# Performance work log

Hardware: AMD Instinct MI355X
Metric: run time of the kernel (lower is better)

The kernel has to match this reference:

```python
import jax, jax.numpy as jnp
import numpy as np

N = 100000   # nodes (word + doc)
E = 1600000  # edges
IN = 256     # in_feats
H = 64       # n_hidden
MH = 64      # mlp_hidden
C = 16       # n_classes


def setup_inputs() -> dict:
    key = jax.random.key(0)
    ks = jax.random.split(key, 12)
    s = lambda f: 1.0 / np.sqrt(f)
    return {
        "x": jax.random.normal(ks[0], (N, IN), jnp.float32),
        "edge_index": jax.random.randint(ks[1], (2, E), 0, N, dtype=jnp.int64),
        "edge_weight": jax.random.uniform(ks[2], (E,), jnp.float32),
        "W1": jax.random.normal(ks[3], (IN, H), jnp.float32) * s(IN),
        "b1": jnp.zeros((H,), jnp.float32),
        "W2": jax.random.normal(ks[4], (H, H), jnp.float32) * s(H),
        "b2": jnp.zeros((H,), jnp.float32),
        "Wm1": jax.random.normal(ks[5], (H, MH), jnp.float32) * s(H),
        "bm1": jnp.zeros((MH,), jnp.float32),
        "Wm2": jax.random.normal(ks[6], (MH, C), jnp.float32) * s(MH),
        "bm2": jnp.zeros((C,), jnp.float32),
    }


def _gcn_norm(edge_index, edge_weight, n):
    # PyG GCNConv: add self-loops (weight 1), symmetric normalization
    loops = jnp.arange(n, dtype=edge_index.dtype)
    src = jnp.concatenate([edge_index[0], loops])
    dst = jnp.concatenate([edge_index[1], loops])
    w = jnp.concatenate([edge_weight, jnp.ones((n,), edge_weight.dtype)])
    deg = jax.ops.segment_sum(w, dst, num_segments=n)
    dinv = jnp.where(deg > 0, jax.lax.rsqrt(deg), 0.0)
    norm = dinv[src] * w * dinv[dst]
    return src, dst, norm


def _gcn_conv(x, W, b, src, dst, norm, n):
    h = x @ W                           # [N, out]
    msg = h[src] * norm[:, None]        # gather + scale, [E+N, out]
    agg = jax.ops.segment_sum(msg, dst, num_segments=n)
    return agg + b


def reference(x, edge_index, edge_weight, W1, b1, W2, b2, Wm1, bm1, Wm2, bm2):
    src, dst, norm = _gcn_norm(edge_index, edge_weight, N)
    # GCN stack (eval mode: dropout is identity)
    h = jax.nn.relu(_gcn_conv(x, W1, b1, src, dst, norm, N))
    h = jax.nn.relu(_gcn_conv(h, W2, b2, src, dst, norm, N))
    # MLP head
    h = jax.nn.relu(h @ Wm1 + bm1)
    logits = h @ Wm2 + bm2
    return jax.nn.softmax(logits, axis=-1)
```

## Files before the change

### kernel.cpp

```cpp
#include <hip/hip_runtime.h>
#include <cstdint>
#include <cstddef>

#define NN 100000
#define NE 1600000
#define IN_F 256
#define HD 64
#define NC 16

#define NT 391
#define NBLK 196
#define EPB 8192
#define CM (NT * NBLK)
#define SCB 75



__global__ __launch_bounds__(256) void k_count(const int* __restrict__ dstA,
                                               int* __restrict__ counts) {
    __shared__ int hist[NT];
    int tid = threadIdx.x;
    for (int t = tid; t < NT; t += 256) hist[t] = 0;
    __syncthreads();
    int base = blockIdx.x * EPB;
#pragma unroll
    for (int i = 0; i < 32; ++i) {
        int e = base + i * 256 + tid;
        if (e < NE) atomicAdd(&hist[dstA[e] >> 8], 1);
    }
    __syncthreads();
    for (int t = tid; t < NT; t += 256)
        counts[t * NBLK + blockIdx.x] = hist[t];
}

__global__ __launch_bounds__(256) void k_scan1(int* __restrict__ c,
                                               int* __restrict__ bsum) {
    __shared__ int ss[256];
    int t = threadIdx.x;
    int base = blockIdx.x * 1024 + t * 4;
    int c0 = (base + 0 < CM) ? c[base + 0] : 0;
    int c1 = (base + 1 < CM) ? c[base + 1] : 0;
    int c2 = (base + 2 < CM) ? c[base + 2] : 0;
    int c3 = (base + 3 < CM) ? c[base + 3] : 0;
    int tsum = c0 + c1 + c2 + c3;
    ss[t] = tsum;
    __syncthreads();
    for (int off = 1; off < 256; off <<= 1) {
        int v = (t >= off) ? ss[t - off] : 0;
        __syncthreads();
        ss[t] += v;
        __syncthreads();
    }
    int excl = ss[t] - tsum;
    if (t == 255) bsum[blockIdx.x] = ss[255];
    if (base + 0 < CM) c[base + 0] = excl;
    if (base + 1 < CM) c[base + 1] = excl + c0;
    if (base + 2 < CM) c[base + 2] = excl + c0 + c1;
    if (base + 3 < CM) c[base + 3] = excl + c0 + c1 + c2;
}

__global__ __launch_bounds__(128) void k_scan2(const int* __restrict__ bsum,
                                               int* __restrict__ bpref) {
    __shared__ int ss[128];
    int t = threadIdx.x;
    int v = (t < SCB) ? bsum[t] : 0;
    ss[t] = v;
    __syncthreads();
    for (int off = 1; off < 128; off <<= 1) {
        int u = (t >= off) ? ss[t - off] : 0;
        __syncthreads();
        ss[t] += u;
        __syncthreads();
    }
    if (t < SCB) bpref[t] = ss[t] - v;
}

__global__ __launch_bounds__(256) void k_scan3(int* __restrict__ c,
                                               const int* __restrict__ bpref) {
    int i = blockIdx.x * 256 + threadIdx.x;
    if (i < CM) c[i] += bpref[i >> 10];
}

template <bool FULL>
__global__ __launch_bounds__(256) void k_fill2(const int* __restrict__ srcA,
                                               const int* __restrict__ dstA,
                                               const float* __restrict__ ew,
                                               const int* __restrict__ counts,
                                               int2* __restrict__ tmp) {
    __shared__ int basel[NT];
    int tid = threadIdx.x;
    for (int t = tid; t < NT; t += 256) basel[t] = counts[t * NBLK + blockIdx.x];
    __syncthreads();
    int eb = blockIdx.x * EPB;
#pragma unroll
    for (int i = 0; i < 32; ++i) {
        int e = eb + i * 256 + tid;
        if (e < NE) {
            int d = dstA[e];
            int pos = atomicAdd(&basel[d >> 8], 1);
            if (FULL)
                tmp[pos] = make_int2(srcA[e] | ((d & 255) << 17),
                                     __float_as_int(ew[e]));
            else
                tmp[pos] = make_int2(e, d & 255);
        }
    }
}

template <bool FULL>
__global__ __launch_bounds__(256) void k_sort(const int* __restrict__ counts,
                                              const int2* __restrict__ tmp,
                                              int2* __restrict__ outP,
                                              int* __restrict__ outE,
                                              int* __restrict__ rowptr,
                                              const float* __restrict__ ew,
                                              float* __restrict__ dinv) {
    __shared__ int hist[256], ss[256], bases[256];
    int tid = threadIdx.x;
    int tile = blockIdx.x;
    int bs = counts[tile * NBLK];
    int be = (tile + 1 < NT) ? counts[(tile + 1) * NBLK] : NE;
    hist[tid] = 0;
    __syncthreads();
    for (int p = bs + tid; p < be; p += 256) {
        int dl = FULL ? ((tmp[p].x >> 17) & 255) : tmp[p].y;
        atomicAdd(&hist[dl], 1);
    }
    __syncthreads();
    int v = hist[tid];
    ss[tid] = v;
    __syncthreads();
    for (int off = 1; off < 256; off <<= 1) {
        int u = (tid >= off) ? ss[tid - off] : 0;
        __syncthreads();
        ss[tid] += u;
        __syncthreads();
    }
    int excl = ss[tid] - v;
    bases[tid] = bs + excl;
    int row = tile * 256 + tid;
    if (row < NN) rowptr[row] = bs + excl;
    if (tile == NT - 1 && tid == 0) rowptr[NN] = NE;
    __syncthreads();
    for (int p = bs + tid; p < be; p += 256) {
        int2 t2 = tmp[p];
        int dl = FULL ? ((t2.x >> 17) & 255) : t2.y;
        int pos = atomicAdd(&bases[dl], 1);
        if (FULL) outP[pos] = t2;
        else      outE[pos] = t2.x;
    }
    __syncthreads();
    if (row < NN) {
        int p0 = bs + excl, p1 = bs + excl + v;
        float s = 1.0f;
        for (int p = p0; p < p1; ++p)
            s += FULL ? __int_as_float(outP[p].y) : ew[outE[p]];
        dinv[row] = rsqrtf(s);
    }
}

template <bool FULL>
__global__ __launch_bounds__(256) void k_agg(const int* __restrict__ rowptr,
                                             const int2* __restrict__ pairsS,
                                             const int* __restrict__ eid,
                                             const int* __restrict__ srcA,
                                             const float* __restrict__ ew,
                                             const float* __restrict__ dinv,
                                             const float* __restrict__ g,
                                             float* __restrict__ agg) {
    int row = blockIdx.x * 4 + (threadIdx.x >> 6);
    int lane = threadIdx.x & 63;
    if (row >= NN) return;
    int p = rowptr[row], pe = rowptr[row + 1];
    float di = dinv[row];
    float acc = g[(size_t)row * HD + lane];
    for (; p + 8 <= pe; p += 8) {
        int   sv[8];
        float wv[8];
        if (FULL) {
#pragma unroll
            for (int i = 0; i < 8; ++i) {
                int2 v = pairsS[p + i];
                sv[i] = v.x & 0x1FFFF;
                wv[i] = __int_as_float(v.y);
            }
        } else {
            int ev[8];
#pragma unroll
            for (int i = 0; i < 8; ++i) ev[i] = eid[p + i];
#pragma unroll
            for (int i = 0; i < 8; ++i) { sv[i] = srcA[ev[i]]; wv[i] = ew[ev[i]]; }
        }
        float gs[8];
#pragma unroll
        for (int i = 0; i < 8; ++i)
            gs[i] = g[(size_t)sv[i] * HD + lane];
#pragma unroll
        for (int i = 0; i < 8; ++i)
            acc = fmaf(wv[i], gs[i], acc);
    }
    for (; p + 4 <= pe; p += 4) {
        if (FULL) {
            int2 v0 = pairsS[p], v1 = pairsS[p + 1],
                 v2 = pairsS[p + 2], v3 = pairsS[p + 3];
            int s0 = v0.x & 0x1FFFF, s1 = v1.x & 0x1FFFF,
                s2 = v2.x & 0x1FFFF, s3 = v3.x & 0x1FFFF;
            float g0 = g[(size_t)s0 * HD + lane];
            float g1 = g[(size_t)s1 * HD + lane];
            float g2 = g[(size_t)s2 * HD + lane];
            float g3 = g[(size_t)s3 * HD + lane];
            acc = fmaf(__int_as_float(v0.y), g0, acc);
            acc = fmaf(__int_as_float(v1.y), g1, acc);
            acc = fmaf(__int_as_float(v2.y), g2, acc);
            acc = fmaf(__int_as_float(v3.y), g3, acc);
        } else {
            int e0 = eid[p], e1 = eid[p + 1], e2 = eid[p + 2], e3 = eid[p + 3];
            int s0 = srcA[e0], s1 = srcA[e1], s2 = srcA[e2], s3 = srcA[e3];
            float g0 = g[(size_t)s0 * HD + lane];
            float g1 = g[(size_t)s1 * HD + lane];
            float g2 = g[(size_t)s2 * HD + lane];
            float g3 = g[(size_t)s3 * HD + lane];
            acc = fmaf(ew[e0], g0, acc);
            acc = fmaf(ew[e1], g1, acc);
            acc = fmaf(ew[e2], g2, acc);
            acc = fmaf(ew[e3], g3, acc);
        }
    }
    for (; p < pe; ++p) {
        if (FULL) {
            int2 v = pairsS[p];
            acc = fmaf(__int_as_float(v.y),
                       g[(size_t)(v.x & 0x1FFFF) * HD + lane], acc);
        } else {
            int e = eid[p];
            acc = fmaf(ew[e], g[(size_t)srcA[e] * HD + lane], acc);
        }
    }
    agg[(size_t)row * HD + lane] = di * acc;
}

template <bool SCALE>
__global__ __launch_bounds__(256, 6) void k_gemm1(const float* __restrict__ x,
                                                  const float* __restrict__ W1,
                                                  const float* __restrict__ dinv,
                                                  float* __restrict__ h0) {
    __shared__ float sX[32][68];
    __shared__ float sW[32][64];
    int tid = threadIdx.x;
    int rs  = tid >> 4;
    int cg  = tid & 15;
    int base = blockIdx.x * 64;

    int f4   = tid >> 5;
    int srow = tid & 31;

    float acc[4][4];
#pragma unroll
    for (int r = 0; r < 4; ++r)
#pragma unroll
        for (int c = 0; c < 4; ++c) acc[r][c] = 0.0f;

    for (int kc = 0; kc < IN_F; kc += 32) {
        __syncthreads();
        {
            const float4* wsrc = (const float4*)(W1 + (size_t)kc * HD);
            float4* wdst = (float4*)&sW[0][0];
            wdst[tid]       = wsrc[tid];
            wdst[256 + tid] = wsrc[256 + tid];
        }
#pragma unroll
        for (int q = 0; q < 2; ++q) {
            int grow = q * 32 + srow;
            int growc = (base + grow < NN) ? (base + grow) : (NN - 1);
            float4 v = *(const float4*)(x + (size_t)growc * IN_F + kc + f4 * 4);
            sX[f4 * 4 + 0][grow] = v.x;
            sX[f4 * 4 + 1][grow] = v.y;
            sX[f4 * 4 + 2][grow] = v.z;
            sX[f4 * 4 + 3][grow] = v.w;
        }
        __syncthreads();
#pragma unroll 4
        for (int k = 0; k < 32; ++k) {
            float xs[4];
            *(float4*)xs = *(const float4*)&sX[k][rs * 4];
            float wv[4];
            *(float4*)wv = *(const float4*)&sW[k][cg * 4];
#pragma unroll
            for (int r = 0; r < 4; ++r) {
                float xj = xs[r];
#pragma unroll
                for (int c = 0; c < 4; ++c) acc[r][c] = fmaf(xj, wv[c], acc[r][c]);
            }
        }
    }
#pragma unroll
    for (int r = 0; r < 4; ++r) {
        int row = base + rs * 4 + r;
        if (row >= NN) continue;
        float di = SCALE ? dinv[row] : 1.0f;
        *(float4*)(h0 + (size_t)row * HD + cg * 4) =
            make_float4(acc[r][0] * di, acc[r][1] * di,
                        acc[r][2] * di, acc[r][3] * di);
    }
}

template <bool BIASRELU, bool SCALEOUT>
__global__ __launch_bounds__(256, 6) void k_gemm64(const float* __restrict__ in,
                                                   const float* __restrict__ bin,
                                                   const float* __restrict__ W,
                                                   const float* __restrict__ bout,
                                                   const float* __restrict__ dinv,
                                                   float* __restrict__ outA) {
    __shared__ float sW[HD * HD];
    __shared__ float sBin[HD];
    int tid = threadIdx.x;
    int rs  = tid >> 4;
    int cg  = tid & 15;
    int base = blockIdx.x * 64;
    int rowc[4];
    bool rv[4];
#pragma unroll
    for (int r = 0; r < 4; ++r) {
        int row = base + rs + 16 * r;
        rv[r] = row < NN;
        rowc[r] = rv[r] ? row : (NN - 1);
    }
    {
        const float4* wsrc = (const float4*)W;
        float4* wdst = (float4*)sW;
#pragma unroll
        for (int q = 0; q < 4; ++q) wdst[q * 256 + tid] = wsrc[q * 256 + tid];
        if (tid < 16) ((float4*)sBin)[tid] = ((const float4*)bin)[tid];
    }
    __syncthreads();
    float acc[4][4];
#pragma unroll
    for (int r = 0; r < 4; ++r)
#pragma unroll
        for (int c = 0; c < 4; ++c) acc[r][c] = 0.0f;

    for (int k4 = 0; k4 < 16; ++k4) {
        float bs[4];
        *(float4*)bs = ((const float4*)sBin)[k4];
        float xs[4][4];
#pragma unroll
        for (int r = 0; r < 4; ++r)
            *(float4*)xs[r] = *(const float4*)(in + (size_t)rowc[r] * HD + k4 * 4);
#pragma unroll
        for (int j = 0; j < 4; ++j) {
            float wv[4];
            *(float4*)wv = *(const float4*)(sW + (k4 * 4 + j) * HD + cg * 4);
#pragma unroll
            for (int r = 0; r < 4; ++r) {
                float hv = fmaxf(xs[r][j] + bs[j], 0.0f);
#pragma unroll
                for (int c = 0; c < 4; ++c) acc[r][c] = fmaf(hv, wv[c], acc[r][c]);
            }
        }
    }
#pragma unroll
    for (int r = 0; r < 4; ++r) {
        if (!rv[r]) continue;
        float* ha = outA + (size_t)rowc[r] * HD + cg * 4;
        if (BIASRELU) {
            float bo[4];
            *(float4*)bo = *(const float4*)(bout + cg * 4);
            *(float4*)ha = make_float4(fmaxf(acc[r][0] + bo[0], 0.0f),
                                       fmaxf(acc[r][1] + bo[1], 0.0f),
                                       fmaxf(acc[r][2] + bo[2], 0.0f),
                                       fmaxf(acc[r][3] + bo[3], 0.0f));
        } else {
            float di = SCALEOUT ? dinv[rowc[r]] : 1.0f;
            *(float4*)ha = make_float4(acc[r][0] * di, acc[r][1] * di,
                                       acc[r][2] * di, acc[r][3] * di);
        }
    }
}

__global__ __launch_bounds__(256) void k_init_fb(float* __restrict__ deg) {
    int i = blockIdx.x * 256 + threadIdx.x;
    if (i < NN) deg[i] = 1.0f;
}
__global__ __launch_bounds__(256) void k_edge_fb(const int* __restrict__ dst,
                                                 const float* __restrict__ ew,
                                                 float* __restrict__ deg) {
    int e = blockIdx.x * 256 + threadIdx.x;
    if (e < NE) atomicAdd(&deg[dst[e]], ew[e]);
}
__global__ __launch_bounds__(256) void k_dinv_fb(float* __restrict__ deg) {
    int i = blockIdx.x * 256 + threadIdx.x;
    if (i < NN) {
        float d = deg[i];
        deg[i] = d > 0.0f ? rsqrtf(d) : 0.0f;
    }
}
__global__ __launch_bounds__(256) void k_selfloop(const float* __restrict__ h,
                                                  const float* __restrict__ dinv,
                                                  float* __restrict__ agg) {
    int i = blockIdx.x * 256 + threadIdx.x;
    if (i >= NN * (HD / 4)) return;
    int row = i / (HD / 4);
    float di = dinv[row];
    float d2 = di * di;
    float4 v = ((const float4*)h)[i];
    ((float4*)agg)[i] = make_float4(v.x * d2, v.y * d2, v.z * d2, v.w * d2);
}
__global__ __launch_bounds__(256) void k_scatter(const int* __restrict__ src,
                                                 const int* __restrict__ dst,
                                                 const float* __restrict__ ew,
                                                 const float* __restrict__ dinv,
                                                 const float* __restrict__ h,
                                                 float* __restrict__ agg) {
    int e = blockIdx.x * 4 + (threadIdx.x >> 6);
    int lane = threadIdx.x & 63;
    if (e >= NE) return;
    int s = src[e];
    int d = dst[e];
    float nrm = dinv[s] * ew[e] * dinv[d];
    float v = h[(size_t)s * HD + lane] * nrm;
    atomicAdd(&agg[(size_t)d * HD + lane], v);
}

__global__ __launch_bounds__(256, 4) void k_out(const float* __restrict__ h3,
                                                const float* __restrict__ Wm2,
                                                const float* __restrict__ bm2,
                                                float* __restrict__ out) {
    __shared__ float sW[HD * NC];
    int tid = threadIdx.x;
    ((float4*)sW)[tid] = ((const float4*)Wm2)[tid];
    __syncthreads();
    int row = blockIdx.x * 256 + tid;
    bool rv = row < NN;
    int rowc = rv ? row : (NN - 1);
    float acc[16];
#pragma unroll
    for (int c = 0; c < 16; ++c) acc[c] = 0.0f;

    for (int k4 = 0; k4 < 16; ++k4) {
        float xs[4];
        *(float4*)xs = *(const float4*)(h3 + (size_t)rowc * HD + k4 * 4);
#pragma unroll
        for (int j = 0; j < 4; ++j) {
            float wv[16];
            const float4* wr4 = (const float4*)(sW + (k4 * 4 + j) * NC);
#pragma unroll
            for (int q = 0; q < 4; ++q) ((float4*)wv)[q] = wr4[q];
            float xj = xs[j];
#pragma unroll
            for (int c = 0; c < 16; ++c) acc[c] = fmaf(xj, wv[c], acc[c]);
        }
    }
    if (!rv) return;
    float bm[16];
#pragma unroll
    for (int q = 0; q < 4; ++q) ((float4*)bm)[q] = ((const float4*)bm2)[q];
    float l[16];
#pragma unroll
    for (int c = 0; c < 16; ++c) l[c] = acc[c] + bm[c];
    float m = l[0];
#pragma unroll
    for (int c = 1; c < 16; ++c) m = fmaxf(m, l[c]);
    float ssum = 0.0f;
#pragma unroll
    for (int c = 0; c < 16; ++c) {
        l[c] = expf(l[c] - m);
        ssum += l[c];
    }
    float inv = 1.0f / ssum;
    float4* op = (float4*)(out + (size_t)rowc * NC);
#pragma unroll
    for (int q = 0; q < 4; ++q)
        op[q] = make_float4(l[q * 4] * inv, l[q * 4 + 1] * inv,
                            l[q * 4 + 2] * inv, l[q * 4 + 3] * inv);
}

extern "C" void kernel_launch(void* const* d_in, const int* in_sizes, int n_in,
                              void* d_out, int out_size, void* d_ws, size_t ws_size,
                              hipStream_t stream) {
    const float* x   = (const float*)d_in[0];
    const int*   ei  = (const int*)d_in[1];
    const float* ew  = (const float*)d_in[2];
    const float* W1  = (const float*)d_in[3];
    const float* b1  = (const float*)d_in[4];
    const float* W2  = (const float*)d_in[5];
    const float* b2  = (const float*)d_in[6];
    const float* Wm1 = (const float*)d_in[7];
    const float* bm1 = (const float*)d_in[8];
    const float* Wm2 = (const float*)d_in[9];
    const float* bm2 = (const float*)d_in[10];
    float* out = (float*)d_out;

    char* base = (char*)d_ws;
    float* dinv   = (float*)base;
    float* A      = (float*)(base + 400128);
    float* B      = (float*)(base + 26000128);
    int*   rowptr = (int*)(base + 51600128);
    int2*  pairsS = (int2*)(base + 52000256);
    int2*  tmp    = (int2*)(base + 400128);
    int*   counts = (int*)(base + 26000128);
    int*   bsum   = (int*)(base + 26000128 + 306544);
    int*   bpref  = (int*)(base + 26000128 + 306944);

    const int* src = ei;
    const int* dst = ei + NE;

    const bool full  = ws_size >= (size_t)64800912;
    const bool douta = !full && ws_size >= (size_t)52000912;
    const int g_node = (NN + 255) / 256;
    const int g_g1   = (NN + 63) / 64;
    const int g_g64  = (NN + 63) / 64;
    const int g_agg  = (NN + 3) / 4;
    const int g_red  = (NN * (HD / 4) + 255) / 256;
    const int g_out  = (NN + 255) / 256;
    int* eid = (int*)d_out;

    if (full || douta) {
        k_count<<<dim3(NBLK), dim3(256), 0, stream>>>(dst, counts);
        k_scan1<<<dim3(SCB), dim3(256), 0, stream>>>(counts, bsum);
        k_scan2<<<dim3(1), dim3(128), 0, stream>>>(bsum, bpref);
        k_scan3<<<dim3((CM + 255) / 256), dim3(256), 0, stream>>>(counts, bpref);
        if (full) {
            k_fill2<true><<<dim3(NBLK), dim3(256), 0, stream>>>(src, dst, ew, counts, tmp);
            k_sort<true><<<dim3(NT), dim3(256), 0, stream>>>(counts, tmp, pairsS, nullptr, rowptr, ew, dinv);
        } else {
            k_fill2<false><<<dim3(NBLK), dim3(256), 0, stream>>>(src, dst, ew, counts, tmp);
            k_sort<false><<<dim3(NT), dim3(256), 0, stream>>>(counts, tmp, nullptr, eid, rowptr, ew, dinv);
        }
        k_gemm1<true><<<dim3(g_g1), dim3(256), 0, stream>>>(x, W1, dinv, A);
        if (full)
            k_agg<true><<<dim3(g_agg), dim3(256), 0, stream>>>(rowptr, pairsS, nullptr, src, ew, dinv, A, B);
        else
            k_agg<false><<<dim3(g_agg), dim3(256), 0, stream>>>(rowptr, nullptr, eid, src, ew, dinv, A, B);
        k_gemm64<false, true><<<dim3(g_g64), dim3(256), 0, stream>>>(B, b1, W2, nullptr, dinv, A);
        if (full)
            k_agg<true><<<dim3(g_agg), dim3(256), 0, stream>>>(rowptr, pairsS, nullptr, src, ew, dinv, A, B);
        else
            k_agg<false><<<dim3(g_agg), dim3(256), 0, stream>>>(rowptr, nullptr, eid, src, ew, dinv, A, B);
        k_gemm64<true, false><<<dim3(g_g64), dim3(256), 0, stream>>>(B, b2, Wm1, bm1, dinv, A);
        k_out<<<dim3(g_out), dim3(256), 0, stream>>>(A, Wm2, bm2, out);
    } else {
        k_init_fb<<<dim3(g_node), dim3(256), 0, stream>>>(dinv);
        k_edge_fb<<<dim3(NE / 256), dim3(256), 0, stream>>>(dst, ew, dinv);
        k_dinv_fb<<<dim3(g_node), dim3(256), 0, stream>>>(dinv);
        k_gemm1<false><<<dim3(g_g1), dim3(256), 0, stream>>>(x, W1, dinv, A);
        k_selfloop<<<dim3(g_red), dim3(256), 0, stream>>>(A, dinv, B);
        k_scatter<<<dim3(NE / 4), dim3(256), 0, stream>>>(src, dst, ew, dinv, A, B);
        k_gemm64<false, false><<<dim3(g_g64), dim3(256), 0, stream>>>(B, b1, W2, nullptr, dinv, A);
        k_selfloop<<<dim3(g_red), dim3(256), 0, stream>>>(A, dinv, B);
        k_scatter<<<dim3(NE / 4), dim3(256), 0, stream>>>(src, dst, ew, dinv, A, B);
        k_gemm64<true, false><<<dim3(g_g64), dim3(256), 0, stream>>>(B, b2, Wm1, bm1, dinv, A);
        k_out<<<dim3(g_out), dim3(256), 0, stream>>>(A, Wm2, bm2, out);
    }
}
```

Baseline: 479.3 us.

## Enlarge gemm1 per-thread tile and stage gemm64 inputs through shared memory

k_gemm1 now runs 128-thread blocks where each thread computes a 4x8 output tile instead of 4x4, so each shared-memory load feeds more FMAs, at the cost of more accumulator registers and fewer threads to hide latency. k_gemm64 now loads the 64x64 input tile once into transposed shared memory with bias+ReLU applied during staging, then runs an inner loop over shared memory. Previously each thread re-read inputs from global memory and recomputed the bias+ReLU per FMA group. The row mapping in gemm64 changes from strided to contiguous rows per thread, and its occupancy hint drops to 4 blocks.

```diff
diff --git a/kernel.cpp b/kernel.cpp
--- a/kernel.cpp
+++ b/kernel.cpp
@@ -240,56 +240,61 @@
 }
 
 template <bool SCALE>
-__global__ __launch_bounds__(256, 6) void k_gemm1(const float* __restrict__ x,
+__global__ __launch_bounds__(128, 3) void k_gemm1(const float* __restrict__ x,
                                                   const float* __restrict__ W1,
                                                   const float* __restrict__ dinv,
                                                   float* __restrict__ h0) {
     __shared__ float sX[32][68];
     __shared__ float sW[32][64];
     int tid = threadIdx.x;
-    int rs  = tid >> 4;
-    int cg  = tid & 15;
+    int rs  = tid >> 3;
+    int cg  = tid & 7;
     int base = blockIdx.x * 64;
 
     int f4   = tid >> 5;
     int srow = tid & 31;
 
-    float acc[4][4];
+    float acc[4][8];
 #pragma unroll
     for (int r = 0; r < 4; ++r)
 #pragma unroll
-        for (int c = 0; c < 4; ++c) acc[r][c] = 0.0f;
+        for (int c = 0; c < 8; ++c) acc[r][c] = 0.0f;
 
     for (int kc = 0; kc < IN_F; kc += 32) {
         __syncthreads();
         {
             const float4* wsrc = (const float4*)(W1 + (size_t)kc * HD);
             float4* wdst = (float4*)&sW[0][0];
-            wdst[tid]       = wsrc[tid];
-            wdst[256 + tid] = wsrc[256 + tid];
+#pragma unroll
+            for (int q = 0; q < 4; ++q) wdst[q * 128 + tid] = wsrc[q * 128 + tid];
         }
 #pragma unroll
         for (int q = 0; q < 2; ++q) {
             int grow = q * 32 + srow;
             int growc = (base + grow < NN) ? (base + grow) : (NN - 1);
-            float4 v = *(const float4*)(x + (size_t)growc * IN_F + kc + f4 * 4);
-            sX[f4 * 4 + 0][grow] = v.x;
-            sX[f4 * 4 + 1][grow] = v.y;
-            sX[f4 * 4 + 2][grow] = v.z;
-            sX[f4 * 4 + 3][grow] = v.w;
+#pragma unroll
+            for (int q2 = 0; q2 < 2; ++q2) {
+                int koff = q2 * 16 + f4 * 4;
+                float4 v = *(const float4*)(x + (size_t)growc * IN_F + kc + koff);
+                sX[koff + 0][grow] = v.x;
+                sX[koff + 1][grow] = v.y;
+                sX[koff + 2][grow] = v.z;
+                sX[koff + 3][grow] = v.w;
+            }
         }
         __syncthreads();
 #pragma unroll 4
         for (int k = 0; k < 32; ++k) {
             float xs[4];
             *(float4*)xs = *(const float4*)&sX[k][rs * 4];
-            float wv[4];
-            *(float4*)wv = *(const float4*)&sW[k][cg * 4];
+            float wv[8];
+            *(float4*)(wv + 0) = *(const float4*)&sW[k][cg * 8];
+            *(float4*)(wv + 4) = *(const float4*)&sW[k][cg * 8 + 4];
 #pragma unroll
             for (int r = 0; r < 4; ++r) {
                 float xj = xs[r];
 #pragma unroll
-                for (int c = 0; c < 4; ++c) acc[r][c] = fmaf(xj, wv[c], acc[r][c]);
+                for (int c = 0; c < 8; ++c) acc[r][c] = fmaf(xj, wv[c], acc[r][c]);
             }
         }
     }
@@ -298,70 +303,78 @@
         int row = base + rs * 4 + r;
         if (row >= NN) continue;
         float di = SCALE ? dinv[row] : 1.0f;
-        *(float4*)(h0 + (size_t)row * HD + cg * 4) =
-            make_float4(acc[r][0] * di, acc[r][1] * di,
-                        acc[r][2] * di, acc[r][3] * di);
+        float* hp = h0 + (size_t)row * HD + cg * 8;
+        *(float4*)(hp + 0) = make_float4(acc[r][0] * di, acc[r][1] * di,
+                                         acc[r][2] * di, acc[r][3] * di);
+        *(float4*)(hp + 4) = make_float4(acc[r][4] * di, acc[r][5] * di,
+                                         acc[r][6] * di, acc[r][7] * di);
     }
 }
 
 template <bool BIASRELU, bool SCALEOUT>
-__global__ __launch_bounds__(256, 6) void k_gemm64(const float* __restrict__ in,
+__global__ __launch_bounds__(256, 4) void k_gemm64(const float* __restrict__ in,
                                                    const float* __restrict__ bin,
                                                    const float* __restrict__ W,
                                                    const float* __restrict__ bout,
                                                    const float* __restrict__ dinv,
                                                    float* __restrict__ outA) {
-    __shared__ float sW[HD * HD];
-    __shared__ float sBin[HD];
+    __shared__ float sIn[64][68];
+    __shared__ float sW[64][64];
     int tid = threadIdx.x;
     int rs  = tid >> 4;
     int cg  = tid & 15;
     int base = blockIdx.x * 64;
-    int rowc[4];
-    bool rv[4];
-#pragma unroll
-    for (int r = 0; r < 4; ++r) {
-        int row = base + rs + 16 * r;
-        rv[r] = row < NN;
-        rowc[r] = rv[r] ? row : (NN - 1);
-    }
+    int f4   = tid >> 5;
+    int srow = tid & 31;
+
     {
         const float4* wsrc = (const float4*)W;
-        float4* wdst = (float4*)sW;
+        float4* wdst = (float4*)&sW[0][0];
 #pragma unroll
         for (int q = 0; q < 4; ++q) wdst[q * 256 + tid] = wsrc[q * 256 + tid];
-        if (tid < 16) ((float4*)sBin)[tid] = ((const float4*)bin)[tid];
-    }
-    __syncthreads();
+    }
+#pragma unroll
+    for (int q2 = 0; q2 < 2; ++q2) {
+        int koff = q2 * 32 + f4 * 4;
+        float4 bb = *(const float4*)(bin + koff);
+#pragma unroll
+        for (int q = 0; q < 2; ++q) {
+            int grow = q * 32 + srow;
+            int growc = (base + grow < NN) ? (base + grow) : (NN - 1);
+            float4 v = *(const float4*)(in + (size_t)growc * HD + koff);
+            sIn[koff + 0][grow] = fmaxf(v.x + bb.x, 0.0f);
+            sIn[koff + 1][grow] = fmaxf(v.y + bb.y, 0.0f);
+            sIn[koff + 2][grow] = fmaxf(v.z + bb.z, 0.0f);
+            sIn[koff + 3][grow] = fmaxf(v.w + bb.w, 0.0f);
+        }
+    }
+    __syncthreads();
+
     float acc[4][4];
 #pragma unroll
     for (int r = 0; r < 4; ++r)
 #pragma unroll
         for (int c = 0; c < 4; ++c) acc[r][c] = 0.0f;
 
-    for (int k4 = 0; k4 < 16; ++k4) {
-        float bs[4];
-        *(float4*)bs = ((const float4*)sBin)[k4];
-        float xs[4][4];
-#pragma unroll
-        for (int r = 0; r < 4; ++r)
-            *(float4*)xs[r] = *(const float4*)(in + (size_t)rowc[r] * HD + k4 * 4);
-#pragma unroll
-        for (int j = 0; j < 4; ++j) {
-            float wv[4];
-            *(float4*)wv = *(const float4*)(sW + (k4 * 4 + j) * HD + cg * 4);
-#pragma unroll
-            for (int r = 0; r < 4; ++r) {
-                float hv = fmaxf(xs[r][j] + bs[j], 0.0f);
-#pragma unroll
-                for (int c = 0; c < 4; ++c) acc[r][c] = fmaf(hv, wv[c], acc[r][c]);
-            }
-        }
-    }
+#pragma unroll 4
+    for (int k = 0; k < HD; ++k) {
+        float xs[4];
+        *(float4*)xs = *(const float4*)&sIn[k][rs * 4];
+        float wv[4];
+        *(float4*)wv = *(const float4*)&sW[k][cg * 4];
+#pragma unroll
+        for (int r = 0; r < 4; ++r) {
+            float hv = xs[r];
+#pragma unroll
+            for (int c = 0; c < 4; ++c) acc[r][c] = fmaf(hv, wv[c], acc[r][c]);
+        }
+    }
+
 #pragma unroll
     for (int r = 0; r < 4; ++r) {
-        if (!rv[r]) continue;
-        float* ha = outA + (size_t)rowc[r] * HD + cg * 4;
+        int row = base + rs * 4 + r;
+        if (row >= NN) continue;
+        float* ha = outA + (size_t)row * HD + cg * 4;
         if (BIASRELU) {
             float bo[4];
             *(float4*)bo = *(const float4*)(bout + cg * 4);
@@ -370,7 +383,7 @@
                                        fmaxf(acc[r][2] + bo[2], 0.0f),
                                        fmaxf(acc[r][3] + bo[3], 0.0f));
         } else {
-            float di = SCALEOUT ? dinv[rowc[r]] : 1.0f;
+            float di = SCALEOUT ? dinv[row] : 1.0f;
             *(float4*)ha = make_float4(acc[r][0] * di, acc[r][1] * di,
                                        acc[r][2] * di, acc[r][3] * di);
         }
@@ -526,7 +539,7 @@
             k_fill2<false><<<dim3(NBLK), dim3(256), 0, stream>>>(src, dst, ew, counts, tmp);
             k_sort<false><<<dim3(NT), dim3(256), 0, stream>>>(counts, tmp, nullptr, eid, rowptr, ew, dinv);
         }
-        k_gemm1<true><<<dim3(g_g1), dim3(256), 0, stream>>>(x, W1, dinv, A);
+        k_gemm1<true><<<dim3(g_g1), dim3(128), 0, stream>>>(x, W1, dinv, A);
         if (full)
             k_agg<true><<<dim3(g_agg), dim3(256), 0, stream>>>(rowptr, pairsS, nullptr, src, ew, dinv, A, B);
         else
@@ -542,7 +555,7 @@
         k_init_fb<<<dim3(g_node), dim3(256), 0, stream>>>(dinv);
         k_edge_fb<<<dim3(NE / 256), dim3(256), 0, stream>>>(dst, ew, dinv);
         k_dinv_fb<<<dim3(g_node), dim3(256), 0, stream>>>(dinv);
-        k_gemm1<false><<<dim3(g_g1), dim3(256), 0, stream>>>(x, W1, dinv, A);
+        k_gemm1<false><<<dim3(g_g1), dim3(128), 0, stream>>>(x, W1, dinv, A);
         k_selfloop<<<dim3(g_red), dim3(256), 0, stream>>>(A, dinv, B);
         k_scatter<<<dim3(NE / 4), dim3(256), 0, stream>>>(src, dst, ew, dinv, A, B);
         k_gemm64<false, false><<<dim3(g_g64), dim3(256), 0, stream>>>(B, b1, W2, nullptr, dinv, A);
```

Result: faster. 457.7 us (-4.5%).
